# Kernel tuning notes

Hardware: AMD Instinct MI355X
Metric: run time of the kernel (lower is better)

## Reference

```python
import jax, jax.numpy as jnp
import numpy as np

N, E, G = 50000, 600000, 64
F_NODE, F_EDGE, F_HAD = 20, 4, 12
D, H, C, L = 128, 4, 32, 3  # hidden, heads, per-head channels, num_layers


def setup_inputs() -> dict:
    key = jax.random.key(0)
    ks = iter(jax.random.split(key, 64))
    nrm = lambda shp, s=0.1: jax.random.normal(next(ks), shp, dtype=jnp.float32) * s
    inp = {
        'x': jax.random.normal(next(ks), (N, F_NODE), dtype=jnp.float32),
        'edge_attr': jax.random.normal(next(ks), (E, F_EDGE), dtype=jnp.float32),
        'haddock_features': jax.random.normal(next(ks), (G, F_HAD), dtype=jnp.float32),
        'edge_index': jax.random.randint(next(ks), (2, E), 0, N, dtype=jnp.int64),
        'batch': (jnp.arange(N, dtype=jnp.int64) * G) // N,  # sorted, all graphs non-empty
        # node embed
        'embed_w': nrm((F_NODE, D)), 'embed_b': jnp.zeros((D,), jnp.float32),
        # GAT layers (stacked over L)
        'gat_lin_w': nrm((L, D, H * C)),
        'gat_att_src': nrm((L, H, C)), 'gat_att_dst': nrm((L, H, C)),
        'gat_edge_w': nrm((L, F_EDGE, H * C)), 'gat_att_edge': nrm((L, H, C)),
        'gat_bias': jnp.zeros((L, H * C), jnp.float32),
        'ln_g': jnp.ones((L, D), jnp.float32), 'ln_b': jnp.zeros((L, D), jnp.float32),
        # haddock processor
        'had_w1': nrm((F_HAD, D)), 'had_b1': jnp.zeros((D,), jnp.float32),
        'had_w2': nrm((D, D)), 'had_b2': jnp.zeros((D,), jnp.float32),
        # interaction head (in = 3*D)
        'int_w1': nrm((3 * D, D)), 'int_b1': jnp.zeros((D,), jnp.float32),
        'int_w2': nrm((D, 64)), 'int_b2': jnp.zeros((64,), jnp.float32),
        'int_w3': nrm((64, 1)), 'int_b3': jnp.zeros((1,), jnp.float32),
        # binding affinity head
        'aff_w1': nrm((3 * D, D)), 'aff_b1': jnp.zeros((D,), jnp.float32),
        'aff_w2': nrm((D, 64)), 'aff_b2': jnp.zeros((64,), jnp.float32),
        'aff_w3': nrm((64, 1)), 'aff_b3': jnp.zeros((1,), jnp.float32),
        # MultiheadAttention with seq_len=1: softmax over 1 key == 1, so output
        # reduces exactly to out_proj(v_proj(x)); q/k projections cancel.
        'mha_v_w': nrm((D, D)), 'mha_v_b': jnp.zeros((D,), jnp.float32),
        'mha_o_w': nrm((D, D)), 'mha_o_b': jnp.zeros((D,), jnp.float32),
    }
    return inp


def _layernorm(x, g, b, eps=1e-5):
    mu = jnp.mean(x, axis=-1, keepdims=True)
    var = jnp.var(x, axis=-1, keepdims=True)
    return (x - mu) * jax.lax.rsqrt(var + eps) * g + b


def _gat_layer(x, src, dst, edge_attr, lin_w, a_src, a_dst, edge_w, a_edge, bias):
    n = x.shape[0]
    h = (x @ lin_w).reshape(n, H, C)                      # [N,H,C]
    alpha_s = jnp.sum(h * a_src, axis=-1)                 # [N,H]
    alpha_d = jnp.sum(h * a_dst, axis=-1)                 # [N,H]
    eemb = (edge_attr @ edge_w).reshape(-1, H, C)         # [E,H,C]
    alpha_e = jnp.sum(eemb * a_edge, axis=-1)             # [E,H]
    alpha = alpha_s[src] + alpha_d[dst] + alpha_e         # [E,H]
    alpha = jax.nn.leaky_relu(alpha, 0.2)
    m = jax.ops.segment_max(alpha, dst, num_segments=n)
    m = jnp.where(jnp.isfinite(m), m, 0.0)
    ex = jnp.exp(alpha - m[dst])
    denom = jax.ops.segment_sum(ex, dst, num_segments=n)
    w = ex / (denom[dst] + 1e-16)                         # segment softmax over dst
    msg = h[src] * w[:, :, None]                          # [E,H,C]
    out = jax.ops.segment_sum(msg, dst, num_segments=n)   # [N,H,C]
    return out.reshape(n, H * C) + bias


def reference(x, edge_attr, haddock_features, embed_w, embed_b,
              gat_lin_w, gat_att_src, gat_att_dst, gat_edge_w, gat_att_edge, gat_bias,
              ln_g, ln_b, had_w1, had_b1, had_w2, had_b2,
              int_w1, int_b1, int_w2, int_b2, int_w3, int_b3,
              aff_w1, aff_b1, aff_w2, aff_b2, aff_w3, aff_b3,
              mha_v_w, mha_v_b, mha_o_w, mha_o_b, edge_index, batch):
    src, dst = edge_index[0], edge_index[1]
    h = jax.nn.relu(x @ embed_w + embed_b)
    for i in range(L):
        res = h
        h = _gat_layer(h, src, dst, edge_attr, gat_lin_w[i], gat_att_src[i],
                       gat_att_dst[i], gat_edge_w[i], gat_att_edge[i], gat_bias[i])
        h = jax.nn.relu(_layernorm(h + res, ln_g[i], ln_b[i]))  # dropout = identity (eval)
    counts = jax.ops.segment_sum(jnp.ones((h.shape[0],), h.dtype), batch, num_segments=G)
    g_mean = jax.ops.segment_sum(h, batch, num_segments=G) / counts[:, None]
    g_max = jax.ops.segment_max(h, batch, num_segments=G)
    graph_embed = jnp.concatenate([g_mean, g_max], axis=1)      # [G,2D]
    had = jax.nn.relu(haddock_features @ had_w1 + had_b1) @ had_w2 + had_b2
    comb = jnp.concatenate([graph_embed, had], axis=1)          # [G,3D]
    z = jax.nn.relu(comb @ int_w1 + int_b1)
    z = jax.nn.relu(z @ int_w2 + int_b2)
    interaction = jax.nn.sigmoid(z @ int_w3 + int_b3)[:, 0]
    z = jax.nn.relu(comb @ aff_w1 + aff_b1)
    z = jax.nn.relu(z @ aff_w2 + aff_b2)
    affinity = (z @ aff_w3 + aff_b3)[:, 0]
    # self-attention over seq_len=1: weights==1, output = out_proj(v_proj(x))
    attn = (h @ mha_v_w + mha_v_b) @ mha_o_w + mha_o_b
    return interaction, affinity, attn, h
```

## Files before the change

### kernel.cpp

```cpp
#include <hip/hip_runtime.h>
#include <hip/hip_bf16.h>

typedef float v4 __attribute__((ext_vector_type(4)));
typedef float f32x4 __attribute__((ext_vector_type(4)));
typedef short bf16x8 __attribute__((ext_vector_type(8)));
typedef unsigned short us8 __attribute__((ext_vector_type(8)));
typedef unsigned short us4 __attribute__((ext_vector_type(4)));

__device__ __forceinline__ unsigned short f2bf(float f) {
    unsigned u = __float_as_uint(f);
    u = (u + 0x7FFFu + ((u >> 16) & 1u)) >> 16;
    return (unsigned short)u;
}
__device__ __forceinline__ float bf2f(unsigned short s) {
    return __uint_as_float(((unsigned)s) << 16);
}

__global__ __launch_bounds__(256) void k_embed(const float* __restrict__ x,
                                               const float* __restrict__ w,
                                               const float* __restrict__ b,
                                               unsigned short* __restrict__ h_bf, int n) {
    int idx = blockIdx.x * 256 + threadIdx.x;
    if (idx >= n * 128) return;
    int node = idx >> 7, j = idx & 127;
    float acc = b[j];
#pragma unroll
    for (int k = 0; k < 20; ++k) acc += x[node * 20 + k] * w[k * 128 + j];
    h_bf[idx] = f2bf(fmaxf(acc, 0.f));
}


__global__ __launch_bounds__(256) void k_hist(const int* __restrict__ ei,
                                              int* __restrict__ cnt, int E_) {
    int e = blockIdx.x * 256 + threadIdx.x;
    if (e < E_) atomicAdd(&cnt[ei[E_ + e]], 1);
}

__global__ __launch_bounds__(256) void k_scan_local(const int* __restrict__ cnt,
                                                    int* __restrict__ ptr,
                                                    int* __restrict__ bsum, int n) {
    __shared__ int s[256];
    int t = threadIdx.x, i = blockIdx.x * 256 + t;
    int v = (i < n) ? cnt[i] : 0;
    s[t] = v;
    __syncthreads();
    for (int o = 1; o < 256; o <<= 1) {
        int x = (t >= o) ? s[t - o] : 0;
        __syncthreads();
        s[t] += x;
        __syncthreads();
    }
    if (i < n) ptr[i] = s[t] - v;
    if (t == 255) bsum[blockIdx.x] = s[255];
}

__global__ __launch_bounds__(256) void k_scan_bsum(int* __restrict__ bsum, int nb) {
    __shared__ int s[256];
    int t = threadIdx.x;
    int v = (t < nb) ? bsum[t] : 0;
    s[t] = v;
    __syncthreads();
    for (int o = 1; o < 256; o <<= 1) {
        int x = (t >= o) ? s[t - o] : 0;
        __syncthreads();
        s[t] += x;
        __syncthreads();
    }
    if (t < nb) bsum[t] = s[t] - v;
}

__global__ __launch_bounds__(256) void k_scan_add(int* __restrict__ ptr,
                                                  const int* __restrict__ bsum,
                                                  int n, int E_) {
    int i = blockIdx.x * 256 + threadIdx.x;
    if (i < n) ptr[i] += bsum[i >> 8];
    if (i == 0) ptr[n] = E_;
}

__global__ __launch_bounds__(256) void k_scatter(const int* __restrict__ ei,
                                                 const float* __restrict__ edge_attr,
                                                 const int* __restrict__ ptr,
                                                 int* __restrict__ cursor,
                                                 int* __restrict__ esrc_s,
                                                 unsigned short* __restrict__ ea_s, int E_) {
    int e = blockIdx.x * 256 + threadIdx.x;
    if (e >= E_) return;
    int d = ei[E_ + e];
    int p = ptr[d] + atomicAdd(&cursor[d], 1);
    esrc_s[p] = ei[e];
    v4 ea = ((const v4*)edge_attr)[e];
    us4 o;
#pragma unroll
    for (int j = 0; j < 4; ++j) o[j] = f2bf(ea[j]);
    *(us4*)&ea_s[(size_t)p * 4] = o;
}

__global__ __launch_bounds__(128) void k_fuse_vo(const float* __restrict__ vw,
                                                 const float* __restrict__ vb,
                                                 const float* __restrict__ ow,
                                                 const float* __restrict__ ob,
                                                 float* __restrict__ Wc,
                                                 float* __restrict__ bc) {
    int k = blockIdx.x, j = threadIdx.x;
    float acc = 0.f;
    for (int m = 0; m < 128; ++m) acc += vw[k * 128 + m] * ow[m * 128 + j];
    Wc[k * 128 + j] = acc;
    if (k == 0) {
        float b = ob[j];
        for (int m = 0; m < 128; ++m) b += vb[m] * ow[m * 128 + j];
        bc[j] = b;
    }
}

__global__ __launch_bounds__(256) void k_pack_w(const float* __restrict__ gat_lin_w,
                                                const float* __restrict__ Wc,
                                                unsigned short* __restrict__ Bpack) {
    int m = blockIdx.y;
    const float* W = (m < 3) ? (gat_lin_w + (size_t)m * 16384) : Wc;
    int idx = blockIdx.x * 256 + threadIdx.x;
    int e = idx & 7, l = (idx >> 3) & 63, kb = (idx >> 9) & 3, c = idx >> 11;
    int k = kb * 32 + ((l >> 4) << 3) + e;
    int col = c * 16 + (l & 15);
    Bpack[(size_t)m * 16384 + idx] = f2bf(W[k * 128 + col]);
}

template <bool ALPHAS, bool OUTF32>
__global__ __launch_bounds__(256) void k_gemm_mfma(
    const unsigned short* __restrict__ A,
    const unsigned short* __restrict__ Bpack,
    const float* __restrict__ bias,
    unsigned short* __restrict__ out_bf,
    float* __restrict__ out_f32,
    const float* __restrict__ avs, const float* __restrict__ avd,
    float* __restrict__ asrc, float* __restrict__ adst, int nn) {
    __shared__ float lds[64][132];
    int tid = threadIdx.x;
    int w = tid >> 6, l = tid & 63;
    int row0 = blockIdx.x * 64;
    int arow = row0 + w * 16 + (l & 15);
    int koff = (l >> 4) * 8;

    bf16x8 a[4];
#pragma unroll
    for (int kb = 0; kb < 4; ++kb)
        a[kb] = *(const bf16x8*)&A[(size_t)arow * 128 + kb * 32 + koff];

    const bf16x8* bp = (const bf16x8*)Bpack;
    f32x4 acc[8];
#pragma unroll
    for (int c = 0; c < 8; ++c) {
        f32x4 z = {0.f, 0.f, 0.f, 0.f};
        acc[c] = z;
#pragma unroll
        for (int kb = 0; kb < 4; ++kb)
            acc[c] = __builtin_amdgcn_mfma_f32_16x16x32_bf16(a[kb], bp[(c * 4 + kb) * 64 + l],
                                                             acc[c], 0, 0, 0);
    }

    int colb = l & 15;
    int rowb = w * 16 + (l >> 4) * 4;
#pragma unroll
    for (int c = 0; c < 8; ++c)
#pragma unroll
        for (int r = 0; r < 4; ++r)
            lds[rowb + r][c * 16 + colb] = acc[c][r];
    __syncthreads();

    int rl = tid >> 2, q = tid & 3;
    int gr = row0 + rl;
    if (gr >= nn) return;
    float v[32];
#pragma unroll
    for (int j = 0; j < 8; ++j)
        *(f32x4*)&v[j * 4] = *(const f32x4*)&lds[rl][q * 32 + j * 4];

    if (ALPHAS) {
        float ps = 0.f, pd = 0.f;
#pragma unroll
        for (int j = 0; j < 32; ++j) {
            ps += v[j] * avs[q * 32 + j];
            pd += v[j] * avd[q * 32 + j];
        }
        asrc[(size_t)gr * 4 + q] = ps;
        adst[(size_t)gr * 4 + q] = pd;
    }
    if (OUTF32) {
#pragma unroll
        for (int j = 0; j < 32; ++j) v[j] += bias[q * 32 + j];
#pragma unroll
        for (int j = 0; j < 8; ++j)
            *(f32x4*)&out_f32[(size_t)gr * 128 + q * 32 + j * 4] = *(f32x4*)&v[j * 4];
    } else {
        us8 o[4];
#pragma unroll
        for (int t = 0; t < 4; ++t)
#pragma unroll
            for (int j = 0; j < 8; ++j) o[t][j] = f2bf(v[t * 8 + j]);
#pragma unroll
        for (int t = 0; t < 4; ++t)
            *(us8*)&out_bf[(size_t)gr * 128 + q * 32 + t * 8] = o[t];
    }
}

template <bool LAST>
__global__ __launch_bounds__(256) void k_node_agg(
    const unsigned short* __restrict__ hl_bf, const int* __restrict__ ptr,
    const int* __restrict__ esrc_s, const unsigned short* __restrict__ ea_s,
    const float* __restrict__ asrc, const float* __restrict__ adst,
    const float* __restrict__ edge_w, const float* __restrict__ a_edge,
    const float* __restrict__ bias, const float* __restrict__ lng,
    const float* __restrict__ lnb, float* __restrict__ h_f32,
    unsigned short* __restrict__ h_bf, int n) {
    __shared__ float aew[16];
    int tid = threadIdx.x;
    if (tid < 16) {
        int k = tid >> 2, hh = tid & 3;
        float s = 0.f;
        for (int c = 0; c < 32; ++c) s += edge_w[k * 128 + hh * 32 + c] * a_edge[hh * 32 + c];
        aew[tid] = s;
    }
    __syncthreads();

    int node = blockIdx.x * 4 + (tid >> 6);
    if (node >= n) return;
    int lane = tid & 63;
    int g = lane >> 4;
    int l16 = lane & 15;
    int c0 = l16 * 8;
    int hh = l16 >> 2;

    float aewc0 = aew[hh], aewc1 = aew[4 + hh], aewc2 = aew[8 + hh], aewc3 = aew[12 + hh];
    int start = ptr[node], end = ptr[node + 1];
    float adn = adst[(size_t)node * 4 + hh];
    us8 res_bf = *(const us8*)&h_bf[(size_t)node * 128 + c0];

    float acc[8] = {};
    float den = 0.f;
    int p = start + g;
    int s0 = (p < end) ? esrc_s[p] : 0;
    int s1 = (p + 4 < end) ? esrc_s[p + 4] : 0;
    for (; p < end; p += 8) {
        bool v1 = (p + 4 < end);
        int sn0 = (p + 8 < end) ? esrc_s[p + 8] : 0;
        int sn1 = (p + 12 < end) ? esrc_s[p + 12] : 0;
        us4 ea0 = *(const us4*)&ea_s[(size_t)p * 4];
        us4 ea1 = *(const us4*)&ea_s[(size_t)(v1 ? (p + 4) : p) * 4];
        us8 hv0 = *(const us8*)&hl_bf[(size_t)s0 * 128 + c0];
        us8 hv1 = *(const us8*)&hl_bf[(size_t)s1 * 128 + c0];
        float as0 = asrc[(size_t)s0 * 4 + hh];
        float as1 = asrc[(size_t)s1 * 4 + hh];
        float a0 = as0 + adn + bf2f(ea0[0]) * aewc0 + bf2f(ea0[1]) * aewc1 +
                   bf2f(ea0[2]) * aewc2 + bf2f(ea0[3]) * aewc3;
        float a1 = as1 + adn + bf2f(ea1[0]) * aewc0 + bf2f(ea1[1]) * aewc1 +
                   bf2f(ea1[2]) * aewc2 + bf2f(ea1[3]) * aewc3;
        a0 = a0 > 0.f ? a0 : 0.2f * a0;
        a1 = a1 > 0.f ? a1 : 0.2f * a1;
        float ex0 = __expf(a0);
        float ex1 = v1 ? __expf(a1) : 0.f;
        den += ex0 + ex1;
#pragma unroll
        for (int j = 0; j < 8; ++j)
            acc[j] += ex0 * bf2f(hv0[j]) + ex1 * bf2f(hv1[j]);
        s0 = sn0; s1 = sn1;
    }

#pragma unroll
    for (int j = 0; j < 8; ++j) {
        acc[j] += __shfl_xor(acc[j], 16);
        acc[j] += __shfl_xor(acc[j], 32);
    }
    den += __shfl_xor(den, 16);
    den += __shfl_xor(den, 32);

    float inv = 1.f / (den + 1e-16f);
    v4 b0 = *(const v4*)&bias[c0];
    v4 b1 = *(const v4*)&bias[c0 + 4];
    float v[8];
#pragma unroll
    for (int j = 0; j < 4; ++j) v[j] = acc[j] * inv + b0[j] + bf2f(res_bf[j]);
#pragma unroll
    for (int j = 0; j < 4; ++j) v[4 + j] = acc[4 + j] * inv + b1[j] + bf2f(res_bf[4 + j]);

    float s = 0.f, sq = 0.f;
#pragma unroll
    for (int j = 0; j < 8; ++j) { s += v[j]; sq += v[j] * v[j]; }
#pragma unroll
    for (int o = 1; o < 16; o <<= 1) { s += __shfl_xor(s, o); sq += __shfl_xor(sq, o); }
    float mu = s * (1.f / 128.f);
    float var = sq * (1.f / 128.f) - mu * mu;
    float rs = rsqrtf(var + 1e-5f);

    if (g == 0) {
        v4 g0 = *(const v4*)&lng[c0];
        v4 g1 = *(const v4*)&lng[c0 + 4];
        v4 lb0 = *(const v4*)&lnb[c0];
        v4 lb1 = *(const v4*)&lnb[c0 + 4];
        v4 o0, o1;
#pragma unroll
        for (int j = 0; j < 4; ++j) o0[j] = fmaxf((v[j] - mu) * rs * g0[j] + lb0[j], 0.f);
#pragma unroll
        for (int j = 0; j < 4; ++j) o1[j] = fmaxf((v[4 + j] - mu) * rs * g1[j] + lb1[j], 0.f);
        us8 ob;
#pragma unroll
        for (int j = 0; j < 4; ++j) ob[j] = f2bf(o0[j]);
#pragma unroll
        for (int j = 0; j < 4; ++j) ob[4 + j] = f2bf(o1[j]);
        *(us8*)&h_bf[(size_t)node * 128 + c0] = ob;
        if (LAST) {
            *(v4*)&h_f32[(size_t)node * 128 + c0] = o0;
            *(v4*)&h_f32[(size_t)node * 128 + c0 + 4] = o1;
        }
    }
}

__device__ __forceinline__ int lower_bound_i(const int* a, int n, int key) {
    int lo = 0, hi = n;
    while (lo < hi) {
        int mid = (lo + hi) >> 1;
        if (a[mid] < key) lo = mid + 1; else hi = mid;
    }
    return lo;
}


__global__ __launch_bounds__(256) void k_pool_part(const unsigned short* __restrict__ h_bf,
                                                   const int* __restrict__ batch,
                                                   float* __restrict__ gsum,
                                                   float* __restrict__ gmax,
                                                   int n, int chunk) {
    int start = blockIdx.x * chunk;
    int end = min(start + chunk, n);
    if (start >= end) return;
    int c0 = (threadIdx.x & 63) * 2;
    int strm = threadIdx.x >> 6;
    float s0 = 0.f, s1 = 0.f, m0 = 0.f, m1 = 0.f;
    int curg = -1;
    for (int node = start + strm; node < end; node += 4) {
        int g = batch[node];
        if (g != curg) {
            if (curg >= 0) {
                atomicAdd(&gsum[curg * 128 + c0], s0);
                atomicAdd(&gsum[curg * 128 + c0 + 1], s1);
                atomicMax((int*)&gmax[curg * 128 + c0], __float_as_int(m0));
                atomicMax((int*)&gmax[curg * 128 + c0 + 1], __float_as_int(m1));
            }
            curg = g; s0 = s1 = 0.f; m0 = m1 = 0.f;
        }
        unsigned u = *(const unsigned*)&h_bf[(size_t)node * 128 + c0];
        float v0 = __uint_as_float(u << 16);
        float v1 = __uint_as_float(u & 0xffff0000u);
        s0 += v0; s1 += v1;
        m0 = fmaxf(m0, v0); m1 = fmaxf(m1, v1);
    }
    if (curg >= 0) {
        atomicAdd(&gsum[curg * 128 + c0], s0);
        atomicAdd(&gsum[curg * 128 + c0 + 1], s1);
        atomicMax((int*)&gmax[curg * 128 + c0], __float_as_int(m0));
        atomicMax((int*)&gmax[curg * 128 + c0 + 1], __float_as_int(m1));
    }
}

__global__ __launch_bounds__(256) void k_graph_out(
    const float* __restrict__ gsum, const float* __restrict__ gmax,
    const int* __restrict__ batch, const float* __restrict__ hf,
    const float* __restrict__ had_w1, const float* __restrict__ had_b1,
    const float* __restrict__ had_w2, const float* __restrict__ had_b2,
    const float* __restrict__ int_w1, const float* __restrict__ int_b1,
    const float* __restrict__ int_w2, const float* __restrict__ int_b2,
    const float* __restrict__ int_w3, const float* __restrict__ int_b3,
    const float* __restrict__ aff_w1, const float* __restrict__ aff_b1,
    const float* __restrict__ aff_w2, const float* __restrict__ aff_b2,
    const float* __restrict__ aff_w3, const float* __restrict__ aff_b3,
    float* __restrict__ inter_out, float* __restrict__ aff_out, int n) {
    __shared__ float comb[384];
    __shared__ float h1[128];
    __shared__ float z1[2][128];
    __shared__ float z2[2][64];
    int g = blockIdx.x, tid = threadIdx.x;
    if (tid < 128) {
        int start = lower_bound_i(batch, n, g);
        int end = lower_bound_i(batch, n, g + 1);
        float cnt = (float)(end - start);
        comb[tid] = gsum[g * 128 + tid] / cnt;
        comb[128 + tid] = gmax[g * 128 + tid];
        float acc = had_b1[tid];
#pragma unroll
        for (int k = 0; k < 12; ++k) acc += hf[g * 12 + k] * had_w1[k * 128 + tid];
        h1[tid] = fmaxf(acc, 0.f);
    }
    __syncthreads();
    if (tid < 128) {
        float a2 = had_b2[tid];
        for (int k = 0; k < 128; ++k) a2 += h1[k] * had_w2[k * 128 + tid];
        comb[256 + tid] = a2;
    }
    __syncthreads();
    int hsel = tid >> 7, j = tid & 127;
    const float* w1 = hsel ? aff_w1 : int_w1;
    const float* b1 = hsel ? aff_b1 : int_b1;
    const float* w2 = hsel ? aff_w2 : int_w2;
    const float* b2 = hsel ? aff_b2 : int_b2;
    const float* w3 = hsel ? aff_w3 : int_w3;
    const float* b3 = hsel ? aff_b3 : int_b3;
    float acc = b1[j];
    for (int k = 0; k < 384; ++k) acc += comb[k] * w1[k * 128 + j];
    z1[hsel][j] = fmaxf(acc, 0.f);
    __syncthreads();
    if (j < 64) {
        float a2 = b2[j];
        for (int k = 0; k < 128; ++k) a2 += z1[hsel][k] * w2[k * 64 + j];
        z2[hsel][j] = fmaxf(a2, 0.f);
    }
    __syncthreads();
    if (j == 0) {
        float a3 = b3[0];
        for (int k = 0; k < 64; ++k) a3 += z2[hsel][k] * w3[k];
        if (hsel) aff_out[g] = a3;
        else inter_out[g] = 1.f / (1.f + __expf(-a3));
    }
}

extern "C" void kernel_launch(void* const* d_in, const int* in_sizes, int n_in,
                              void* d_out, int out_size, void* d_ws, size_t ws_size,
                              hipStream_t stream) {
    const float* x = (const float*)d_in[0];
    const float* edge_attr = (const float*)d_in[1];
    const float* haddock = (const float*)d_in[2];
    const int* ei = (const int*)d_in[3];
    const int* batch = (const int*)d_in[4];
    const float* embed_w = (const float*)d_in[5];
    const float* embed_b = (const float*)d_in[6];
    const float* gat_lin_w = (const float*)d_in[7];
    const float* gat_att_src = (const float*)d_in[8];
    const float* gat_att_dst = (const float*)d_in[9];
    const float* gat_edge_w = (const float*)d_in[10];
    const float* gat_att_edge = (const float*)d_in[11];
    const float* gat_bias = (const float*)d_in[12];
    const float* ln_g = (const float*)d_in[13];
    const float* ln_b = (const float*)d_in[14];
    const float* had_w1 = (const float*)d_in[15];
    const float* had_b1 = (const float*)d_in[16];
    const float* had_w2 = (const float*)d_in[17];
    const float* had_b2 = (const float*)d_in[18];
    const float* int_w1 = (const float*)d_in[19];
    const float* int_b1 = (const float*)d_in[20];
    const float* int_w2 = (const float*)d_in[21];
    const float* int_b2 = (const float*)d_in[22];
    const float* int_w3 = (const float*)d_in[23];
    const float* int_b3 = (const float*)d_in[24];
    const float* aff_w1 = (const float*)d_in[25];
    const float* aff_b1 = (const float*)d_in[26];
    const float* aff_w2 = (const float*)d_in[27];
    const float* aff_b2 = (const float*)d_in[28];
    const float* aff_w3 = (const float*)d_in[29];
    const float* aff_b3 = (const float*)d_in[30];
    const float* mha_v_w = (const float*)d_in[31];
    const float* mha_v_b = (const float*)d_in[32];
    const float* mha_o_w = (const float*)d_in[33];
    const float* mha_o_b = (const float*)d_in[34];

    const int N_ = in_sizes[0] / 20;
    const int E_ = in_sizes[1] / 4;
    const int G_ = in_sizes[2] / 12;
    const int Npad = (N_ + 63) & ~63;

    float* out_f = (float*)d_out;
    float* inter_out = out_f;
    float* aff_out = out_f + G_;
    float* attn_out = out_f + 2 * G_;
    float* h_buf = attn_out + (size_t)N_ * 128;

    unsigned short* h_bf = (unsigned short*)d_ws;
    unsigned short* hl_bf = h_bf + (size_t)Npad * 128;
    unsigned short* Bpack = hl_bf + (size_t)Npad * 128;
    unsigned short* ea_s = Bpack + 4 * 16384;
    float* Wc = (float*)(ea_s + (size_t)E_ * 4);
    float* bc = Wc + 16384;
    float* asrc = bc + 128;
    float* adst = asrc + (size_t)N_ * 4;
    float* gsum = adst + (size_t)N_ * 4;
    float* gmax = gsum + (size_t)G_ * 128;
    int* cnt = (int*)(gmax + (size_t)G_ * 128);
    int* cursor = cnt + N_;
    int* ptr = cursor + N_;
    int* bsum = ptr + N_ + 4;
    int* esrc_s = bsum + 256;

    const int nb_scan = (N_ + 255) / 256;
    const int POOL_BLOCKS = 2048;
    const int chunk = (N_ + POOL_BLOCKS - 1) / POOL_BLOCKS;
    const int gemm_blocks = (N_ + 63) / 64;

    k_embed<<<(N_ * 128 + 255) / 256, 256, 0, stream>>>(x, embed_w, embed_b, h_bf, N_);

    hipMemsetAsync(cnt, 0, (size_t)2 * N_ * sizeof(int), stream);
    k_hist<<<(E_ + 255) / 256, 256, 0, stream>>>(ei, cnt, E_);
    k_scan_local<<<nb_scan, 256, 0, stream>>>(cnt, ptr, bsum, N_);
    k_scan_bsum<<<1, 256, 0, stream>>>(bsum, nb_scan);
    k_scan_add<<<nb_scan, 256, 0, stream>>>(ptr, bsum, N_, E_);
    k_scatter<<<(E_ + 255) / 256, 256, 0, stream>>>(ei, edge_attr, ptr, cursor,
                                                    esrc_s, ea_s, E_);

    k_fuse_vo<<<128, 128, 0, stream>>>(mha_v_w, mha_v_b, mha_o_w, mha_o_b, Wc, bc);
    k_pack_w<<<dim3(64, 4), 256, 0, stream>>>(gat_lin_w, Wc, Bpack);
    hipMemsetAsync(gsum, 0, (size_t)2 * G_ * 128 * sizeof(float), stream);

    for (int i = 0; i < 3; ++i) {
        k_gemm_mfma<true, false><<<gemm_blocks, 256, 0, stream>>>(
            h_bf, Bpack + (size_t)i * 16384, nullptr, hl_bf, nullptr,
            gat_att_src + i * 128, gat_att_dst + i * 128, asrc, adst, N_);
        if (i < 2)
            k_node_agg<false><<<(N_ + 3) / 4, 256, 0, stream>>>(
                hl_bf, ptr, esrc_s, ea_s, asrc, adst,
                gat_edge_w + (size_t)i * 512, gat_att_edge + i * 128,
                gat_bias + i * 128, ln_g + i * 128, ln_b + i * 128, h_buf, h_bf, N_);
        else
            k_node_agg<true><<<(N_ + 3) / 4, 256, 0, stream>>>(
                hl_bf, ptr, esrc_s, ea_s, asrc, adst,
                gat_edge_w + (size_t)i * 512, gat_att_edge + i * 128,
                gat_bias + i * 128, ln_g + i * 128, ln_b + i * 128, h_buf, h_bf, N_);
    }

    k_pool_part<<<POOL_BLOCKS, 256, 0, stream>>>(h_bf, batch, gsum, gmax, N_, chunk);
    k_graph_out<<<G_, 256, 0, stream>>>(gsum, gmax, batch, haddock,
                                        had_w1, had_b1, had_w2, had_b2,
                                        int_w1, int_b1, int_w2, int_b2, int_w3, int_b3,
                                        aff_w1, aff_b1, aff_w2, aff_b2, aff_w3, aff_b3,
                                        inter_out, aff_out, N_);
    k_gemm_mfma<false, true><<<gemm_blocks, 256, 0, stream>>>(
        h_bf, Bpack + (size_t)3 * 16384, bc, nullptr, attn_out,
        nullptr, nullptr, nullptr, nullptr, N_);
}
```

Baseline: 394.3 us.

## Merge setup kernels and memsets into one launch; fuse graph head with final GEMM

```diff
diff --git a/kernel.cpp b/kernel.cpp
--- a/kernel.cpp
+++ b/kernel.cpp
@@ -16,17 +16,53 @@
     return __uint_as_float(((unsigned)s) << 16);
 }
 
-__global__ __launch_bounds__(256) void k_embed(const float* __restrict__ x,
-                                               const float* __restrict__ w,
-                                               const float* __restrict__ b,
-                                               unsigned short* __restrict__ h_bf, int n) {
-    int idx = blockIdx.x * 256 + threadIdx.x;
-    if (idx >= n * 128) return;
-    int node = idx >> 7, j = idx & 127;
-    float acc = b[j];
-#pragma unroll
-    for (int k = 0; k < 20; ++k) acc += x[node * 20 + k] * w[k * 128 + j];
-    h_bf[idx] = f2bf(fmaxf(acc, 0.f));
+__global__ __launch_bounds__(256) void k_setup(
+    const float* __restrict__ x, const float* __restrict__ embed_w,
+    const float* __restrict__ embed_b, unsigned short* __restrict__ h_bf,
+    int* __restrict__ cnt_cursor,
+    const float* __restrict__ gat_lin_w,
+    const float* __restrict__ vw, const float* __restrict__ vb,
+    const float* __restrict__ ow, const float* __restrict__ ob,
+    unsigned short* __restrict__ Bpack, float* __restrict__ bc,
+    float* __restrict__ gzero,
+    int n, int nbA, int nbB) {
+    int b = blockIdx.x, tid = threadIdx.x;
+    if (b < nbA) {
+        int idx = b * 256 + tid;
+        if (idx >= n * 128) return;
+        int node = idx >> 7, j = idx & 127;
+        float acc = embed_b[j];
+#pragma unroll
+        for (int k = 0; k < 20; ++k) acc += x[node * 20 + k] * embed_w[k * 128 + j];
+        h_bf[idx] = f2bf(fmaxf(acc, 0.f));
+    } else if (b < nbA + nbB) {
+        int idx = (b - nbA) * 256 + tid;
+        if (idx < 2 * n) cnt_cursor[idx] = 0;
+    } else if (b < nbA + nbB + 256) {
+        int pb = b - nbA - nbB;
+        int m = pb >> 6;
+        int idx = (pb & 63) * 256 + tid;
+        int e = idx & 7, l = (idx >> 3) & 63, kb = (idx >> 9) & 3, c = idx >> 11;
+        int k = kb * 32 + ((l >> 4) << 3) + e;
+        int col = c * 16 + (l & 15);
+        float val;
+        if (m < 3) {
+            val = gat_lin_w[(size_t)m * 16384 + k * 128 + col];
+        } else {
+            val = 0.f;
+            for (int m2 = 0; m2 < 128; ++m2) val += vw[k * 128 + m2] * ow[m2 * 128 + col];
+        }
+        Bpack[(size_t)m * 16384 + idx] = f2bf(val);
+    } else if (b == nbA + nbB + 256) {
+        if (tid < 128) {
+            float bv = ob[tid];
+            for (int m2 = 0; m2 < 128; ++m2) bv += vb[m2] * ow[m2 * 128 + tid];
+            bc[tid] = bv;
+        }
+    } else {
+        int idx = (b - (nbA + nbB + 257)) * 256 + tid;
+        if (idx < 16384) gzero[idx] = 0.f;
+    }
 }
 
 
@@ -93,35 +129,6 @@
 #pragma unroll
     for (int j = 0; j < 4; ++j) o[j] = f2bf(ea[j]);
     *(us4*)&ea_s[(size_t)p * 4] = o;
-}
-
-__global__ __launch_bounds__(128) void k_fuse_vo(const float* __restrict__ vw,
-                                                 const float* __restrict__ vb,
-                                                 const float* __restrict__ ow,
-                                                 const float* __restrict__ ob,
-                                                 float* __restrict__ Wc,
-                                                 float* __restrict__ bc) {
-    int k = blockIdx.x, j = threadIdx.x;
-    float acc = 0.f;
-    for (int m = 0; m < 128; ++m) acc += vw[k * 128 + m] * ow[m * 128 + j];
-    Wc[k * 128 + j] = acc;
-    if (k == 0) {
-        float b = ob[j];
-        for (int m = 0; m < 128; ++m) b += vb[m] * ow[m * 128 + j];
-        bc[j] = b;
-    }
-}
-
-__global__ __launch_bounds__(256) void k_pack_w(const float* __restrict__ gat_lin_w,
-                                                const float* __restrict__ Wc,
-                                                unsigned short* __restrict__ Bpack) {
-    int m = blockIdx.y;
-    const float* W = (m < 3) ? (gat_lin_w + (size_t)m * 16384) : Wc;
-    int idx = blockIdx.x * 256 + threadIdx.x;
-    int e = idx & 7, l = (idx >> 3) & 63, kb = (idx >> 9) & 3, c = idx >> 11;
-    int k = kb * 32 + ((l >> 4) << 3) + e;
-    int col = c * 16 + (l & 15);
-    Bpack[(size_t)m * 16384 + idx] = f2bf(W[k * 128 + col]);
 }
 
 template <bool ALPHAS, bool OUTF32>
@@ -360,7 +367,7 @@
     }
 }
 
-__global__ __launch_bounds__(256) void k_graph_out(
+__global__ __launch_bounds__(256) void k_tail(
     const float* __restrict__ gsum, const float* __restrict__ gmax,
     const int* __restrict__ batch, const float* __restrict__ hf,
     const float* __restrict__ had_w1, const float* __restrict__ had_b1,
@@ -371,53 +378,103 @@
     const float* __restrict__ aff_w1, const float* __restrict__ aff_b1,
     const float* __restrict__ aff_w2, const float* __restrict__ aff_b2,
     const float* __restrict__ aff_w3, const float* __restrict__ aff_b3,
-    float* __restrict__ inter_out, float* __restrict__ aff_out, int n) {
-    __shared__ float comb[384];
-    __shared__ float h1[128];
-    __shared__ float z1[2][128];
-    __shared__ float z2[2][64];
-    int g = blockIdx.x, tid = threadIdx.x;
-    if (tid < 128) {
-        int start = lower_bound_i(batch, n, g);
-        int end = lower_bound_i(batch, n, g + 1);
-        float cnt = (float)(end - start);
-        comb[tid] = gsum[g * 128 + tid] / cnt;
-        comb[128 + tid] = gmax[g * 128 + tid];
-        float acc = had_b1[tid];
-#pragma unroll
-        for (int k = 0; k < 12; ++k) acc += hf[g * 12 + k] * had_w1[k * 128 + tid];
-        h1[tid] = fmaxf(acc, 0.f);
-    }
+    float* __restrict__ inter_out, float* __restrict__ aff_out,
+    const unsigned short* __restrict__ A, const unsigned short* __restrict__ Bpack,
+    const float* __restrict__ bias, float* __restrict__ out_f32,
+    int G_, int nn, int n) {
+    __shared__ float lds[64][132];
+    int tid = threadIdx.x;
+    if ((int)blockIdx.x < G_) {
+        __shared__ float comb[384];
+        __shared__ float h1[128];
+        __shared__ float z1[2][128];
+        __shared__ float z2[2][64];
+        int g = blockIdx.x;
+        if (tid < 128) {
+            int start = lower_bound_i(batch, n, g);
+            int end = lower_bound_i(batch, n, g + 1);
+            float cntf = (float)(end - start);
+            comb[tid] = gsum[g * 128 + tid] / cntf;
+            comb[128 + tid] = gmax[g * 128 + tid];
+            float acc = had_b1[tid];
+#pragma unroll
+            for (int k = 0; k < 12; ++k) acc += hf[g * 12 + k] * had_w1[k * 128 + tid];
+            h1[tid] = fmaxf(acc, 0.f);
+        }
+        __syncthreads();
+        if (tid < 128) {
+            float a2 = had_b2[tid];
+            for (int k = 0; k < 128; ++k) a2 += h1[k] * had_w2[k * 128 + tid];
+            comb[256 + tid] = a2;
+        }
+        __syncthreads();
+        int hsel = tid >> 7, j = tid & 127;
+        const float* w1 = hsel ? aff_w1 : int_w1;
+        const float* b1 = hsel ? aff_b1 : int_b1;
+        const float* w2 = hsel ? aff_w2 : int_w2;
+        const float* b2 = hsel ? aff_b2 : int_b2;
+        const float* w3 = hsel ? aff_w3 : int_w3;
+        const float* b3 = hsel ? aff_b3 : int_b3;
+        float acc = b1[j];
+        for (int k = 0; k < 384; ++k) acc += comb[k] * w1[k * 128 + j];
+        z1[hsel][j] = fmaxf(acc, 0.f);
+        __syncthreads();
+        if (j < 64) {
+            float a2 = b2[j];
+            for (int k = 0; k < 128; ++k) a2 += z1[hsel][k] * w2[k * 64 + j];
+            z2[hsel][j] = fmaxf(a2, 0.f);
+        }
+        __syncthreads();
+        if (j == 0) {
+            float a3 = b3[0];
+            for (int k = 0; k < 64; ++k) a3 += z2[hsel][k] * w3[k];
+            if (hsel) aff_out[g] = a3;
+            else inter_out[g] = 1.f / (1.f + __expf(-a3));
+        }
+        return;
+    }
+    int w = tid >> 6, l = tid & 63;
+    int row0 = ((int)blockIdx.x - G_) * 64;
+    int arow = row0 + w * 16 + (l & 15);
+    int koff = (l >> 4) * 8;
+
+    bf16x8 a[4];
+#pragma unroll
+    for (int kb = 0; kb < 4; ++kb)
+        a[kb] = *(const bf16x8*)&A[(size_t)arow * 128 + kb * 32 + koff];
+
+    const bf16x8* bp = (const bf16x8*)Bpack;
+    f32x4 acc[8];
+#pragma unroll
+    for (int c = 0; c < 8; ++c) {
+        f32x4 z = {0.f, 0.f, 0.f, 0.f};
+        acc[c] = z;
+#pragma unroll
+        for (int kb = 0; kb < 4; ++kb)
+            acc[c] = __builtin_amdgcn_mfma_f32_16x16x32_bf16(a[kb], bp[(c * 4 + kb) * 64 + l],
+                                                             acc[c], 0, 0, 0);
+    }
+    int colb = l & 15;
+    int rowb = w * 16 + (l >> 4) * 4;
+#pragma unroll
+    for (int c = 0; c < 8; ++c)
+#pragma unroll
+        for (int r = 0; r < 4; ++r)
+            lds[rowb + r][c * 16 + colb] = acc[c][r];
     __syncthreads();
-    if (tid < 128) {
-        float a2 = had_b2[tid];
-        for (int k = 0; k < 128; ++k) a2 += h1[k] * had_w2[k * 128 + tid];
-        comb[256 + tid] = a2;
-    }
-    __syncthreads();
-    int hsel = tid >> 7, j = tid & 127;
-    const float* w1 = hsel ? aff_w1 : int_w1;
-    const float* b1 = hsel ? aff_b1 : int_b1;
-    const float* w2 = hsel ? aff_w2 : int_w2;
-    const float* b2 = hsel ? aff_b2 : int_b2;
-    const float* w3 = hsel ? aff_w3 : int_w3;
-    const float* b3 = hsel ? aff_b3 : int_b3;
-    float acc = b1[j];
-    for (int k = 0; k < 384; ++k) acc += comb[k] * w1[k * 128 + j];
-    z1[hsel][j] = fmaxf(acc, 0.f);
-    __syncthreads();
-    if (j < 64) {
-        float a2 = b2[j];
-        for (int k = 0; k < 128; ++k) a2 += z1[hsel][k] * w2[k * 64 + j];
-        z2[hsel][j] = fmaxf(a2, 0.f);
-    }
-    __syncthreads();
-    if (j == 0) {
-        float a3 = b3[0];
-        for (int k = 0; k < 64; ++k) a3 += z2[hsel][k] * w3[k];
-        if (hsel) aff_out[g] = a3;
-        else inter_out[g] = 1.f / (1.f + __expf(-a3));
-    }
+
+    int rl = tid >> 2, q = tid & 3;
+    int gr = row0 + rl;
+    if (gr >= nn) return;
+    float v[32];
+#pragma unroll
+    for (int j = 0; j < 8; ++j)
+        *(f32x4*)&v[j * 4] = *(const f32x4*)&lds[rl][q * 32 + j * 4];
+#pragma unroll
+    for (int j = 0; j < 32; ++j) v[j] += bias[q * 32 + j];
+#pragma unroll
+    for (int j = 0; j < 8; ++j)
+        *(f32x4*)&out_f32[(size_t)gr * 128 + q * 32 + j * 4] = *(f32x4*)&v[j * 4];
 }
 
 extern "C" void kernel_launch(void* const* d_in, const int* in_sizes, int n_in,
@@ -474,8 +531,7 @@
     unsigned short* hl_bf = h_bf + (size_t)Npad * 128;
     unsigned short* Bpack = hl_bf + (size_t)Npad * 128;
     unsigned short* ea_s = Bpack + 4 * 16384;
-    float* Wc = (float*)(ea_s + (size_t)E_ * 4);
-    float* bc = Wc + 16384;
+    float* bc = (float*)(ea_s + (size_t)E_ * 4);
     float* asrc = bc + 128;
     float* adst = asrc + (size_t)N_ * 4;
     float* gsum = adst + (size_t)N_ * 4;
@@ -491,19 +547,20 @@
     const int chunk = (N_ + POOL_BLOCKS - 1) / POOL_BLOCKS;
     const int gemm_blocks = (N_ + 63) / 64;
 
-    k_embed<<<(N_ * 128 + 255) / 256, 256, 0, stream>>>(x, embed_w, embed_b, h_bf, N_);
-
-    hipMemsetAsync(cnt, 0, (size_t)2 * N_ * sizeof(int), stream);
+    const int nbA = (N_ * 128 + 255) / 256;
+    const int nbB = (2 * N_ + 255) / 256;
+    const int nbE = 64;
+    k_setup<<<nbA + nbB + 256 + 1 + nbE, 256, 0, stream>>>(
+        x, embed_w, embed_b, h_bf, cnt,
+        gat_lin_w, mha_v_w, mha_v_b, mha_o_w, mha_o_b,
+        Bpack, bc, gsum, N_, nbA, nbB);
+
     k_hist<<<(E_ + 255) / 256, 256, 0, stream>>>(ei, cnt, E_);
     k_scan_local<<<nb_scan, 256, 0, stream>>>(cnt, ptr, bsum, N_);
     k_scan_bsum<<<1, 256, 0, stream>>>(bsum, nb_scan);
     k_scan_add<<<nb_scan, 256, 0, stream>>>(ptr, bsum, N_, E_);
     k_scatter<<<(E_ + 255) / 256, 256, 0, stream>>>(ei, edge_attr, ptr, cursor,
                                                     esrc_s, ea_s, E_);
-
-    k_fuse_vo<<<128, 128, 0, stream>>>(mha_v_w, mha_v_b, mha_o_w, mha_o_b, Wc, bc);
-    k_pack_w<<<dim3(64, 4), 256, 0, stream>>>(gat_lin_w, Wc, Bpack);
-    hipMemsetAsync(gsum, 0, (size_t)2 * G_ * 128 * sizeof(float), stream);
 
     for (int i = 0; i < 3; ++i) {
         k_gemm_mfma<true, false><<<gemm_blocks, 256, 0, stream>>>(
@@ -522,12 +579,11 @@
     }
 
     k_pool_part<<<POOL_BLOCKS, 256, 0, stream>>>(h_bf, batch, gsum, gmax, N_, chunk);
-    k_graph_out<<<G_, 256, 0, stream>>>(gsum, gmax, batch, haddock,
-                                        had_w1, had_b1, had_w2, had_b2,
-                                        int_w1, int_b1, int_w2, int_b2, int_w3, int_b3,
-                                        aff_w1, aff_b1, aff_w2, aff_b2, aff_w3, aff_b3,
-                                        inter_out, aff_out, N_);
-    k_gemm_mfma<false, true><<<gemm_blocks, 256, 0, stream>>>(
-        h_bf, Bpack + (size_t)3 * 16384, bc, nullptr, attn_out,
-        nullptr, nullptr, nullptr, nullptr, N_);
-}
+    k_tail<<<G_ + gemm_blocks, 256, 0, stream>>>(
+        gsum, gmax, batch, haddock,
+        had_w1, had_b1, had_w2, had_b2,
+        int_w1, int_b1, int_w2, int_b2, int_w3, int_b3,
+        aff_w1, aff_b1, aff_w2, aff_b2, aff_w3, aff_b3,
+        inter_out, aff_out,
+        h_bf, Bpack + (size_t)3 * 16384, bc, attn_out, G_, N_, N_);
+}
```

Result: faster. 358.2 us (-9.2%).
